# Kernel tuning notes

Hardware: AMD Instinct MI355X
Metric: run time of the kernel (lower is better)

Reference implementation:

```python
import jax, jax.numpy as jnp
import numpy as np

B, S, HID = 2, 2048, 2048
NH, NKV, DH = 16, 4, 128
EPS = 1e-6

def rotate_half(x):
    x1, x2 = x[..., : x.shape[-1] // 2], x[..., x.shape[-1] // 2 :]
    return jnp.concatenate((-x2, x1), axis=-1)

def rms_norm(x, w):
    var = jnp.mean(jnp.square(x), axis=-1, keepdims=True)
    return w * (x * jax.lax.rsqrt(var + EPS))

def setup_inputs() -> dict:
    key = jax.random.key(0)
    ks = jax.random.split(key, 8)
    hidden_states = jax.random.normal(ks[0], (B, S, HID), dtype=jnp.float32)
    # causal additive mask, broadcastable to [B, H, S, S]
    causal = jnp.tril(jnp.ones((S, S), dtype=bool))
    attention_mask = jnp.where(causal, 0.0, -1e9).astype(jnp.float32)[None, None]
    # RoPE tables: [1, S, 1, DH] to broadcast over (B, S, H, DH)
    inv_freq = 1.0 / (10000.0 ** (np.arange(0, DH, 2, dtype=np.float32) / DH))
    t = np.arange(S, dtype=np.float32)
    freqs = np.einsum('s,d->sd', t, inv_freq)
    emb = np.concatenate([freqs, freqs], axis=-1)  # [S, DH]
    cos = jnp.asarray(np.cos(emb))[None, :, None, :]
    sin = jnp.asarray(np.sin(emb))[None, :, None, :]
    std = 0.02
    Wq = jax.random.normal(ks[1], (HID, NH * DH), dtype=jnp.float32) * std
    Wk = jax.random.normal(ks[2], (HID, NKV * DH), dtype=jnp.float32) * std
    Wv = jax.random.normal(ks[3], (HID, NKV * DH), dtype=jnp.float32) * std
    Wo = jax.random.normal(ks[4], (NH * DH, HID), dtype=jnp.float32) * std
    q_norm_w = jnp.ones((DH,), dtype=jnp.float32)
    k_norm_w = jnp.ones((DH,), dtype=jnp.float32)
    return dict(hidden_states=hidden_states, attention_mask=attention_mask,
                cos=cos, sin=sin, Wq=Wq, Wk=Wk, Wv=Wv, Wo=Wo,
                q_norm_w=q_norm_w, k_norm_w=k_norm_w)

def reference(hidden_states, attention_mask, cos, sin, Wq, Wk, Wv, Wo, q_norm_w, k_norm_w):
    b, s, _ = hidden_states.shape
    q = (hidden_states @ Wq).reshape(b, s, NH, DH)
    k = (hidden_states @ Wk).reshape(b, s, NKV, DH)
    v = (hidden_states @ Wv).reshape(b, s, NKV, DH)
    # per-head RMSNorm on q/k
    q = rms_norm(q, q_norm_w)
    k = rms_norm(k, k_norm_w)
    # RoPE
    q = q * cos + rotate_half(q) * sin
    k = k * cos + rotate_half(k) * sin
    # GQA: repeat kv heads
    groups = NH // NKV
    k = jnp.repeat(k, groups, axis=2)
    v = jnp.repeat(v, groups, axis=2)
    scale = 1.0 / jnp.sqrt(jnp.asarray(DH, dtype=q.dtype))
    scores = jnp.einsum('bqhd,bkhd->bhqk', q, k) * scale  # [B,H,S,S]
    scores = scores + attention_mask
    probs = jax.nn.softmax(scores, axis=-1)
    out = jnp.einsum('bhqk,bkhd->bqhd', probs, v)
    out = out.reshape(b, s, NH * DH)
    return out @ Wo
```

## Files before the change

kernel.cpp:

```cpp
#include <hip/hip_runtime.h>
#include <hip/hip_bf16.h>
#include <stdint.h>


typedef __attribute__((ext_vector_type(8))) short short8;
typedef __attribute__((ext_vector_type(4))) float floatx4;
typedef __hip_bfloat16 bf16_t;

#define MFMA16x16(a, b, c) __builtin_amdgcn_mfma_f32_16x16x32_bf16(a, b, c, 0, 0, 0)

__device__ __forceinline__ void async_copy16(const void* g, void* l) {
  __builtin_amdgcn_global_load_lds(
      (const __attribute__((address_space(1))) void*)g,
      (__attribute__((address_space(3))) void*)l, 16, 0, 0);
}

__device__ __forceinline__ unsigned short bf16bits(float x) {
  bf16_t h = __float2bfloat16(x);
  return *reinterpret_cast<unsigned short*>(&h);
}

__global__ __launch_bounds__(256) void convbf_kernel(const float* __restrict__ in,
                                                     bf16_t* __restrict__ out, int n4) {
  int i = blockIdx.x * 256 + threadIdx.x;
  if (i < n4) {
    const float4 v = reinterpret_cast<const float4*>(in)[i];
    ushort4 o;
    o.x = bf16bits(v.x); o.y = bf16bits(v.y); o.z = bf16bits(v.z); o.w = bf16bits(v.w);
    reinterpret_cast<ushort4*>(out)[i] = o;
  }
}

__global__ __launch_bounds__(256) void wtrans_kernel(const float* __restrict__ W,
                                                     bf16_t* __restrict__ Wt, int N, int roff) {
  __shared__ float t[32][33];
  int k0 = blockIdx.y * 32, n0 = blockIdx.x * 32;
#pragma unroll
  for (int j = 0; j < 4; ++j)
    t[threadIdx.y + j * 8][threadIdx.x] =
        W[(size_t)(k0 + threadIdx.y + j * 8) * N + n0 + threadIdx.x];
  __syncthreads();
#pragma unroll
  for (int j = 0; j < 4; ++j) {
    int n = n0 + threadIdx.y + j * 8, k = k0 + threadIdx.x;
    Wt[(size_t)(roff + n) * 2048 + k] = __float2bfloat16(t[threadIdx.x][threadIdx.y + j * 8]);
  }
}

template <int OBF>
__global__ __launch_bounds__(256, 3) void gemm_bt_kernel(const bf16_t* __restrict__ A,
                                                         const bf16_t* __restrict__ Bt,
                                                         void* __restrict__ Cv,
                                                         int K, int ldc) {
  __shared__ __align__(16) char smem[32768];
  const int tid = threadIdx.x;
  const int wave = tid >> 6, lane = tid & 63;
  const int wr = wave >> 1, wc = wave & 1;
  const int l16 = lane & 15, lhi = lane >> 4;

  const int nwg = gridDim.x * gridDim.y;
  const int orig = blockIdx.y * gridDim.x + blockIdx.x;
  const int swz = (orig & 7) * (nwg >> 3) + (orig >> 3);
  const int bn = (swz % gridDim.x) * 128;
  const int bm = (swz / gridDim.x) * 128;

  floatx4 acc[4][4] = {};

  for (int k0 = 0; k0 < K; k0 += 64) {
    __syncthreads();
#pragma unroll
    for (int i = 0; i < 4; ++i) {
      int chunk = i * 4 + wave;
      unsigned p = (unsigned)chunk * 1024u + (unsigned)lane * 16u;
      unsigned row = p >> 7;
      unsigned colg = (p & 127u) ^ ((row & 7u) << 4);
      const char* gA = (const char*)(A + (size_t)(bm + row) * K + k0) + colg;
      async_copy16(gA, smem + (size_t)chunk * 1024);
      const char* gB = (const char*)(Bt + (size_t)(bn + row) * K + k0) + colg;
      async_copy16(gB, smem + 16384 + (size_t)chunk * 1024);
    }
    __syncthreads();
#pragma unroll
    for (int kk = 0; kk < 2; ++kk) {
      short8 fa[4], fb[4];
#pragma unroll
      for (int mi = 0; mi < 4; ++mi) {
        unsigned row = wr * 64 + mi * 16 + l16;
        unsigned off = row * 128u + kk * 64u + lhi * 16u;
        off ^= (row & 7u) << 4;
        fa[mi] = *(const short8*)(smem + off);
      }
#pragma unroll
      for (int ni = 0; ni < 4; ++ni) {
        unsigned row = wc * 64 + ni * 16 + l16;
        unsigned off = row * 128u + kk * 64u + lhi * 16u;
        off ^= (row & 7u) << 4;
        fb[ni] = *(const short8*)(smem + 16384 + off);
      }
#pragma unroll
      for (int mi = 0; mi < 4; ++mi)
#pragma unroll
        for (int ni = 0; ni < 4; ++ni)
          acc[mi][ni] = MFMA16x16(fa[mi], fb[ni], acc[mi][ni]);
    }
  }
#pragma unroll
  for (int mi = 0; mi < 4; ++mi)
#pragma unroll
    for (int ni = 0; ni < 4; ++ni)
#pragma unroll
      for (int r = 0; r < 4; ++r) {
        int row = bm + wr * 64 + mi * 16 + lhi * 4 + r;
        int col = bn + wc * 64 + ni * 16 + l16;
        if (OBF)
          ((bf16_t*)Cv)[(size_t)row * ldc + col] = __float2bfloat16(acc[mi][ni][r]);
        else
          ((float*)Cv)[(size_t)row * ldc + col] = acc[mi][ni][r];
      }
}

__global__ __launch_bounds__(256) void qknorm_rope_kernel(
    const bf16_t* __restrict__ Cqkv, const float* __restrict__ cosT,
    const float* __restrict__ sinT, const float* __restrict__ qw,
    const float* __restrict__ kw, bf16_t* __restrict__ Qa, bf16_t* __restrict__ Ka) {
  int wave = threadIdx.x >> 6, lane = threadIdx.x & 63;
  int task = blockIdx.x * 4 + wave;
  int unit = task % 20;
  int row = task / 20;
  int b = row >> 11, s = row & 2047;
  const bf16_t* src;
  const float* w;
  bf16_t* dst;
  float sc;
  if (unit < 16) {
    src = Cqkv + (size_t)row * 3072 + unit * 128;
    w = qw;
    dst = Qa + ((size_t)(b * 16 + unit) * 2048 + s) * 128;
    sc = 0.088388347648318447f;
  } else {
    int kh = unit - 16;
    src = Cqkv + (size_t)row * 3072 + 2048 + kh * 128;
    w = kw;
    dst = Ka + ((size_t)(b * 4 + kh) * 2048 + s) * 128;
    sc = 1.0f;
  }
  float x1 = __bfloat162float(src[lane]), x2 = __bfloat162float(src[lane + 64]);
  float ss = x1 * x1 + x2 * x2;
#pragma unroll
  for (int off = 1; off < 64; off <<= 1) ss += __shfl_xor(ss, off, 64);
  float inv = rsqrtf(ss * (1.f / 128.f) + 1e-6f);
  x1 = x1 * inv * w[lane];
  x2 = x2 * inv * w[lane + 64];
  float c1 = cosT[(size_t)s * 128 + lane], c2 = cosT[(size_t)s * 128 + lane + 64];
  float s1 = sinT[(size_t)s * 128 + lane], s2 = sinT[(size_t)s * 128 + lane + 64];
  dst[lane] = __float2bfloat16((x1 * c1 - x2 * s1) * sc);
  dst[lane + 64] = __float2bfloat16((x2 * c2 + x1 * s2) * sc);
}

__global__ __launch_bounds__(256) void vtrans_kernel(const bf16_t* __restrict__ Cqkv,
                                                     bf16_t* __restrict__ Vt) {
  __shared__ bf16_t t[32][33];
  int bk = blockIdx.z;
  int b = bk >> 2, kh = bk & 3;
  int s0 = blockIdx.x * 32, d0 = blockIdx.y * 32;
  const bf16_t* src = Cqkv + (size_t)(b * 2048) * 3072 + 2560 + kh * 128;
#pragma unroll
  for (int j = 0; j < 4; ++j)
    t[threadIdx.y + j * 8][threadIdx.x] =
        src[(size_t)(s0 + threadIdx.y + j * 8) * 3072 + d0 + threadIdx.x];
  __syncthreads();
  bf16_t* dst = Vt + (size_t)(b * 4 + kh) * 128 * 2048;
#pragma unroll
  for (int j = 0; j < 4; ++j) {
    int d = d0 + threadIdx.y + j * 8, s = s0 + threadIdx.x;
    dst[(size_t)d * 2048 + s] = t[threadIdx.x][threadIdx.y + j * 8];
  }
}

__device__ __forceinline__ unsigned swz_row(unsigned row) {
  return (((row & 7u) ^ ((row >> 3) << 1)) & 7u) << 4;
}

__global__ __launch_bounds__(256, 2) void flash_kernel(const bf16_t* __restrict__ Qa,
                                                       const bf16_t* __restrict__ Ka,
                                                       const bf16_t* __restrict__ Vt,
                                                       bf16_t* __restrict__ attnO) {
  __shared__ __align__(16) char smem[65536];
  const int tid = threadIdx.x;
  const int wave = tid >> 6, lane = tid & 63;
  const int l16 = lane & 15, lhi = lane >> 4;
  const int bid = blockIdx.x;
  const int bh = bid & 31;
  const int ib = bid >> 5;
  const int qb = (ib < 8) ? (15 - ib) : (ib - 8);
  const int h = bh & 15, b = bh >> 4;
  const int kh = h >> 2;
  const int q0b = qb << 7;
  const int q0w = q0b + wave * 32;

  const bf16_t* Qb = Qa + ((size_t)bh * 2048 + q0w) * 128;
  const bf16_t* Kb = Ka + (size_t)(b * 4 + kh) * 2048 * 128;
  const bf16_t* Vb = Vt + (size_t)(b * 4 + kh) * 128 * 2048;

  char* Kl = smem;
  char* Vl = smem + 32768;

  short8 qf[2][4];
#pragma unroll
  for (int rt = 0; rt < 2; ++rt)
#pragma unroll
    for (int kk = 0; kk < 4; ++kk)
      qf[rt][kk] = *(const short8*)(Qb + (size_t)(rt * 16 + l16) * 128 + kk * 32 + lhi * 8);

  short8 onesf;
#pragma unroll
  for (int j = 0; j < 8; ++j) onesf[j] = (short)0x3F80;

  floatx4 o[2][8] = {};
  floatx4 lsum[2] = {};
  short8 pf[2][4];
  float m[2] = {-1e30f, -1e30f};

  const float THR = 8.0f;
  const int nch = qb + 1;

  auto stageK = [&](int key0) {
#pragma unroll
    for (int it = 0; it < 8; ++it) {
      unsigned p = (unsigned)(it * 4 + wave) * 1024u + (unsigned)lane * 16u;
      unsigned row = p >> 8;
      unsigned gcol = (p & 255u) ^ swz_row(row);
      async_copy16((const char*)(Kb + (size_t)(key0 + row) * 128) + gcol,
                   Kl + (size_t)(it * 4 + wave) * 1024);
    }
  };
  auto stageV = [&](int key0) {
#pragma unroll
    for (int it = 0; it < 8; ++it) {
      unsigned p = (unsigned)(it * 4 + wave) * 1024u + (unsigned)lane * 16u;
      unsigned row = p >> 8;
      unsigned gcol = (p & 255u) ^ swz_row(row);
      async_copy16((const char*)(Vb + (size_t)row * 2048 + key0) + gcol,
                   Vl + (size_t)(it * 4 + wave) * 1024);
    }
  };

  stageK(0);
  stageV(0);
  __syncthreads();

  for (int c = 0; c < nch; ++c) {
    const int kc0 = c << 7;

    floatx4 s[2][8] = {};
    __builtin_amdgcn_s_setprio(1);
#pragma unroll
    for (int g = 0; g < 8; ++g) {
      unsigned row = (unsigned)(l16 >> 2) * 8u + (unsigned)((g & 1) * 4) +
                     (unsigned)(l16 & 3) + (unsigned)((g >> 1) * 32);
      unsigned base = row * 256u;
      unsigned px = swz_row(row);
#pragma unroll
      for (int kk = 0; kk < 4; ++kk) {
        short8 kf = *(const short8*)(Kl + base + (((unsigned)(kk * 64 + lhi * 16)) ^ px));
        s[0][g] = MFMA16x16(kf, qf[0][kk], s[0][g]);
        s[1][g] = MFMA16x16(kf, qf[1][kk], s[1][g]);
      }
    }
    __builtin_amdgcn_s_setprio(0);

    const bool needMask = (kc0 + 128 > q0w);
#pragma unroll
    for (int rt = 0; rt < 2; ++rt) {
      const int qrow = q0w + rt * 16 + l16;
      if (needMask) {
#pragma unroll
        for (int g = 0; g < 8; ++g)
#pragma unroll
          for (int r = 0; r < 4; ++r) {
            int key = kc0 + lhi * 8 + (g & 1) * 4 + r + (g >> 1) * 32;
            if (key > qrow) s[rt][g][r] = -1e9f;
          }
      }
      float mx = s[rt][0][0];
#pragma unroll
      for (int g = 0; g < 8; ++g)
#pragma unroll
        for (int r = 0; r < 4; ++r) mx = fmaxf(mx, s[rt][g][r]);
      mx = fmaxf(mx, __shfl_xor(mx, 16, 64));
      mx = fmaxf(mx, __shfl_xor(mx, 32, 64));
      bool grow = mx > m[rt] + THR;
      if (__any(grow)) {
        float mn = fmaxf(m[rt], mx);
        float corr = __expf(m[rt] - mn);
        m[rt] = mn;
#pragma unroll
        for (int r = 0; r < 4; ++r) {
          float co = __shfl(corr, lhi * 4 + r, 64);
          lsum[rt][r] *= co;
#pragma unroll
          for (int f = 0; f < 8; ++f) o[rt][f][r] *= co;
        }
      }
#pragma unroll
      for (int ks = 0; ks < 4; ++ks) {
        union { unsigned u[4]; short8 v; } pk;
#pragma unroll
        for (int half = 0; half < 2; ++half) {
          int g = ks * 2 + half;
          float p0 = __expf(s[rt][g][0] - m[rt]);
          float p1 = __expf(s[rt][g][1] - m[rt]);
          float p2 = __expf(s[rt][g][2] - m[rt]);
          float p3 = __expf(s[rt][g][3] - m[rt]);
          pk.u[half * 2] = (unsigned)bf16bits(p0) | ((unsigned)bf16bits(p1) << 16);
          pk.u[half * 2 + 1] = (unsigned)bf16bits(p2) | ((unsigned)bf16bits(p3) << 16);
        }
        pf[rt][ks] = pk.v;
      }
    }

    __syncthreads();

    if (c + 1 < nch) stageK(kc0 + 128);

    __builtin_amdgcn_s_setprio(1);
#pragma unroll
    for (int ks = 0; ks < 4; ++ks) {
#pragma unroll
      for (int f = 0; f < 8; ++f) {
        unsigned row = (unsigned)(f * 16 + l16);
        short8 vf = *(const short8*)(Vl + row * 256u +
                                     (((unsigned)(ks * 64 + lhi * 16)) ^ swz_row(row)));
        o[0][f] = MFMA16x16(pf[0][ks], vf, o[0][f]);
        o[1][f] = MFMA16x16(pf[1][ks], vf, o[1][f]);
      }
      lsum[0] = MFMA16x16(pf[0][ks], onesf, lsum[0]);
      lsum[1] = MFMA16x16(pf[1][ks], onesf, lsum[1]);
    }
    __builtin_amdgcn_s_setprio(0);

    __syncthreads();

    if (c + 1 < nch) stageV(kc0 + 128);
  }

#pragma unroll
  for (int rt = 0; rt < 2; ++rt)
#pragma unroll
    for (int r = 0; r < 4; ++r) {
      float inv = 1.f / lsum[rt][r];
      int row = q0w + rt * 16 + lhi * 4 + r;
      size_t base = ((size_t)(b * 2048) + row) * 2048 + h * 128;
#pragma unroll
      for (int f = 0; f < 8; ++f)
        attnO[base + f * 16 + l16] = __float2bfloat16(o[rt][f][r] * inv);
    }
}

extern "C" void kernel_launch(void* const* d_in, const int* in_sizes, int n_in,
                              void* d_out, int out_size, void* d_ws, size_t ws_size,
                              hipStream_t stream) {
  const float* hs = (const float*)d_in[0];
  const float* cosT = (const float*)d_in[2];
  const float* sinT = (const float*)d_in[3];
  const float* Wq = (const float*)d_in[4];
  const float* Wk = (const float*)d_in[5];
  const float* Wv = (const float*)d_in[6];
  const float* Wo = (const float*)d_in[7];
  const float* qw = (const float*)d_in[8];
  const float* kw = (const float*)d_in[9];
  float* out = (float*)d_out;

  char* ws = (char*)d_ws;
  size_t off = 0;
  auto alloc = [&](size_t bytes) {
    char* p = ws + off;
    off += (bytes + 255) & ~(size_t)255;
    return p;
  };
  bf16_t* hsb  = (bf16_t*)alloc((size_t)4096 * 2048 * 2);
  bf16_t* wqkv = (bf16_t*)alloc((size_t)3072 * 2048 * 2);
  bf16_t* wot  = (bf16_t*)alloc((size_t)2048 * 2048 * 2);
  bf16_t* cqkv = (bf16_t*)alloc((size_t)4096 * 3072 * 2);
  bf16_t* qa   = (bf16_t*)alloc((size_t)2 * 16 * 2048 * 128 * 2);
  bf16_t* ka   = (bf16_t*)alloc((size_t)2 * 4 * 2048 * 128 * 2);
  bf16_t* vt   = (bf16_t*)alloc((size_t)2 * 4 * 2048 * 128 * 2);
  bf16_t* attn = (bf16_t*)cqkv;

  convbf_kernel<<<8192, 256, 0, stream>>>(hs, hsb, 2097152);
  dim3 tb(32, 8);
  wtrans_kernel<<<dim3(64, 64), tb, 0, stream>>>(Wq, wqkv, 2048, 0);
  wtrans_kernel<<<dim3(16, 64), tb, 0, stream>>>(Wk, wqkv, 512, 2048);
  wtrans_kernel<<<dim3(16, 64), tb, 0, stream>>>(Wv, wqkv, 512, 2560);
  wtrans_kernel<<<dim3(64, 64), tb, 0, stream>>>(Wo, wot, 2048, 0);
  gemm_bt_kernel<1><<<dim3(24, 32), 256, 0, stream>>>(hsb, wqkv, cqkv, 2048, 3072);
  qknorm_rope_kernel<<<20480, 256, 0, stream>>>(cqkv, cosT, sinT, qw, kw, qa, ka);
  vtrans_kernel<<<dim3(64, 4, 8), tb, 0, stream>>>(cqkv, vt);
  flash_kernel<<<512, 256, 0, stream>>>(qa, ka, vt, attn);
  gemm_bt_kernel<0><<<dim3(16, 32), 256, 0, stream>>>(attn, wot, out, 2048, 2048);
}
```

Measured before the change: 216.5 us.

## Halve flash attention tiles to 64 queries/keys, use exp2 with folded log2e scale

The flash kernel now gives each block 64 query rows (16 per wave) and 64-key chunks, doubling the grid to 1024 blocks and halving shared memory to 32KB, with a new load-balancing map from block index to query block. The softmax scale folds in log2(e) so exponentials use the hardware exp2 directly, and the lazy-rescale threshold is raised to match the base-2 domain. This is meant to improve occupancy and load balance and cut the cost of each exponential. In exchange it halves K/V reuse per block, adds more barriers and chunk iterations, and loads more K/V in total.

After: 188.4 us (median of 2 runs). 1.15x faster.

```diff
diff --git a/kernel.cpp b/kernel.cpp
--- a/kernel.cpp
+++ b/kernel.cpp
@@ -18,6 +18,10 @@
 __device__ __forceinline__ unsigned short bf16bits(float x) {
   bf16_t h = __float2bfloat16(x);
   return *reinterpret_cast<unsigned short*>(&h);
+}
+
+__device__ __forceinline__ float fast_exp2(float x) {
+  return __builtin_amdgcn_exp2f(x);
 }
 
 __global__ __launch_bounds__(256) void convbf_kernel(const float* __restrict__ in,
@@ -136,7 +140,7 @@
     src = Cqkv + (size_t)row * 3072 + unit * 128;
     w = qw;
     dst = Qa + ((size_t)(b * 16 + unit) * 2048 + s) * 128;
-    sc = 0.088388347648318447f;
+    sc = 0.127517432f;
   } else {
     int kh = unit - 16;
     src = Cqkv + (size_t)row * 3072 + 2048 + kh * 128;
@@ -181,52 +185,53 @@
   return (((row & 7u) ^ ((row >> 3) << 1)) & 7u) << 4;
 }
 
+__device__ __constant__ unsigned char kQbMap[32] = {
+    31, 30, 29, 28, 27, 26, 25, 24,  0, 1, 2, 3, 4, 5, 6, 7,
+    23, 22, 21, 20, 19, 18, 17, 16,  8, 9, 10, 11, 12, 13, 14, 15};
+
 __global__ __launch_bounds__(256, 2) void flash_kernel(const bf16_t* __restrict__ Qa,
                                                        const bf16_t* __restrict__ Ka,
                                                        const bf16_t* __restrict__ Vt,
                                                        bf16_t* __restrict__ attnO) {
-  __shared__ __align__(16) char smem[65536];
+  __shared__ __align__(16) char smem[32768];
   const int tid = threadIdx.x;
   const int wave = tid >> 6, lane = tid & 63;
   const int l16 = lane & 15, lhi = lane >> 4;
   const int bid = blockIdx.x;
   const int bh = bid & 31;
-  const int ib = bid >> 5;
-  const int qb = (ib < 8) ? (15 - ib) : (ib - 8);
+  const int qb = kQbMap[bid >> 5];
   const int h = bh & 15, b = bh >> 4;
   const int kh = h >> 2;
-  const int q0b = qb << 7;
-  const int q0w = q0b + wave * 32;
+  const int q0b = qb << 6;
+  const int q0w = q0b + wave * 16;
 
   const bf16_t* Qb = Qa + ((size_t)bh * 2048 + q0w) * 128;
   const bf16_t* Kb = Ka + (size_t)(b * 4 + kh) * 2048 * 128;
   const bf16_t* Vb = Vt + (size_t)(b * 4 + kh) * 128 * 2048;
 
   char* Kl = smem;
-  char* Vl = smem + 32768;
-
-  short8 qf[2][4];
-#pragma unroll
-  for (int rt = 0; rt < 2; ++rt)
-#pragma unroll
-    for (int kk = 0; kk < 4; ++kk)
-      qf[rt][kk] = *(const short8*)(Qb + (size_t)(rt * 16 + l16) * 128 + kk * 32 + lhi * 8);
+  char* Vl = smem + 16384;
+
+  short8 qf[4];
+#pragma unroll
+  for (int kk = 0; kk < 4; ++kk)
+    qf[kk] = *(const short8*)(Qb + (size_t)l16 * 128 + kk * 32 + lhi * 8);
 
   short8 onesf;
 #pragma unroll
   for (int j = 0; j < 8; ++j) onesf[j] = (short)0x3F80;
 
-  floatx4 o[2][8] = {};
-  floatx4 lsum[2] = {};
-  short8 pf[2][4];
-  float m[2] = {-1e30f, -1e30f};
-
-  const float THR = 8.0f;
+  floatx4 o[8] = {};
+  floatx4 lsum = {};
+  short8 pf[2];
+  float m = -1e30f;
+
+  const float THR = 11.5f;
   const int nch = qb + 1;
 
   auto stageK = [&](int key0) {
 #pragma unroll
-    for (int it = 0; it < 8; ++it) {
+    for (int it = 0; it < 4; ++it) {
       unsigned p = (unsigned)(it * 4 + wave) * 1024u + (unsigned)lane * 16u;
       unsigned row = p >> 8;
       unsigned gcol = (p & 255u) ^ swz_row(row);
@@ -236,10 +241,10 @@
   };
   auto stageV = [&](int key0) {
 #pragma unroll
-    for (int it = 0; it < 8; ++it) {
+    for (int it = 0; it < 4; ++it) {
       unsigned p = (unsigned)(it * 4 + wave) * 1024u + (unsigned)lane * 16u;
-      unsigned row = p >> 8;
-      unsigned gcol = (p & 255u) ^ swz_row(row);
+      unsigned row = p >> 7;
+      unsigned gcol = (p & 127u) ^ swz_row(row);
       async_copy16((const char*)(Vb + (size_t)row * 2048 + key0) + gcol,
                    Vl + (size_t)(it * 4 + wave) * 1024);
     }
@@ -250,12 +255,12 @@
   __syncthreads();
 
   for (int c = 0; c < nch; ++c) {
-    const int kc0 = c << 7;
-
-    floatx4 s[2][8] = {};
+    const int kc0 = c << 6;
+
+    floatx4 s[4] = {};
     __builtin_amdgcn_s_setprio(1);
 #pragma unroll
-    for (int g = 0; g < 8; ++g) {
+    for (int g = 0; g < 4; ++g) {
       unsigned row = (unsigned)(l16 >> 2) * 8u + (unsigned)((g & 1) * 4) +
                      (unsigned)(l16 & 3) + (unsigned)((g >> 1) * 32);
       unsigned base = row * 256u;
@@ -263,98 +268,89 @@
 #pragma unroll
       for (int kk = 0; kk < 4; ++kk) {
         short8 kf = *(const short8*)(Kl + base + (((unsigned)(kk * 64 + lhi * 16)) ^ px));
-        s[0][g] = MFMA16x16(kf, qf[0][kk], s[0][g]);
-        s[1][g] = MFMA16x16(kf, qf[1][kk], s[1][g]);
+        s[g] = MFMA16x16(kf, qf[kk], s[g]);
       }
     }
     __builtin_amdgcn_s_setprio(0);
 
-    const bool needMask = (kc0 + 128 > q0w);
-#pragma unroll
-    for (int rt = 0; rt < 2; ++rt) {
-      const int qrow = q0w + rt * 16 + l16;
-      if (needMask) {
-#pragma unroll
-        for (int g = 0; g < 8; ++g)
-#pragma unroll
-          for (int r = 0; r < 4; ++r) {
-            int key = kc0 + lhi * 8 + (g & 1) * 4 + r + (g >> 1) * 32;
-            if (key > qrow) s[rt][g][r] = -1e9f;
-          }
-      }
-      float mx = s[rt][0][0];
-#pragma unroll
-      for (int g = 0; g < 8; ++g)
-#pragma unroll
-        for (int r = 0; r < 4; ++r) mx = fmaxf(mx, s[rt][g][r]);
-      mx = fmaxf(mx, __shfl_xor(mx, 16, 64));
-      mx = fmaxf(mx, __shfl_xor(mx, 32, 64));
-      bool grow = mx > m[rt] + THR;
-      if (__any(grow)) {
-        float mn = fmaxf(m[rt], mx);
-        float corr = __expf(m[rt] - mn);
-        m[rt] = mn;
+    const int qrow = q0w + l16;
+    if (kc0 + 64 > q0w) {
+#pragma unroll
+      for (int g = 0; g < 4; ++g)
 #pragma unroll
         for (int r = 0; r < 4; ++r) {
-          float co = __shfl(corr, lhi * 4 + r, 64);
-          lsum[rt][r] *= co;
-#pragma unroll
-          for (int f = 0; f < 8; ++f) o[rt][f][r] *= co;
+          int key = kc0 + lhi * 8 + (g & 1) * 4 + r + (g >> 1) * 32;
+          if (key > qrow) s[g][r] = -1e9f;
         }
-      }
-#pragma unroll
-      for (int ks = 0; ks < 4; ++ks) {
-        union { unsigned u[4]; short8 v; } pk;
-#pragma unroll
-        for (int half = 0; half < 2; ++half) {
-          int g = ks * 2 + half;
-          float p0 = __expf(s[rt][g][0] - m[rt]);
-          float p1 = __expf(s[rt][g][1] - m[rt]);
-          float p2 = __expf(s[rt][g][2] - m[rt]);
-          float p3 = __expf(s[rt][g][3] - m[rt]);
-          pk.u[half * 2] = (unsigned)bf16bits(p0) | ((unsigned)bf16bits(p1) << 16);
-          pk.u[half * 2 + 1] = (unsigned)bf16bits(p2) | ((unsigned)bf16bits(p3) << 16);
-        }
-        pf[rt][ks] = pk.v;
-      }
+    }
+    float m0 = fmaxf(fmaxf(s[0][0], s[0][1]), fmaxf(s[0][2], s[0][3]));
+    float m1 = fmaxf(fmaxf(s[1][0], s[1][1]), fmaxf(s[1][2], s[1][3]));
+    float m2 = fmaxf(fmaxf(s[2][0], s[2][1]), fmaxf(s[2][2], s[2][3]));
+    float m3 = fmaxf(fmaxf(s[3][0], s[3][1]), fmaxf(s[3][2], s[3][3]));
+    float mx = fmaxf(fmaxf(m0, m1), fmaxf(m2, m3));
+    mx = fmaxf(mx, __shfl_xor(mx, 16, 64));
+    mx = fmaxf(mx, __shfl_xor(mx, 32, 64));
+    bool grow = mx > m + THR;
+    if (__any(grow)) {
+      float mn = fmaxf(m, mx);
+      float corr = fast_exp2(m - mn);
+      m = mn;
+#pragma unroll
+      for (int r = 0; r < 4; ++r) {
+        float co = __shfl(corr, lhi * 4 + r, 64);
+        lsum[r] *= co;
+#pragma unroll
+        for (int f = 0; f < 8; ++f) o[f][r] *= co;
+      }
+    }
+#pragma unroll
+    for (int ks = 0; ks < 2; ++ks) {
+      union { unsigned u[4]; short8 v; } pk;
+#pragma unroll
+      for (int half = 0; half < 2; ++half) {
+        int g = ks * 2 + half;
+        float p0 = fast_exp2(s[g][0] - m);
+        float p1 = fast_exp2(s[g][1] - m);
+        float p2 = fast_exp2(s[g][2] - m);
+        float p3 = fast_exp2(s[g][3] - m);
+        pk.u[half * 2] = (unsigned)bf16bits(p0) | ((unsigned)bf16bits(p1) << 16);
+        pk.u[half * 2 + 1] = (unsigned)bf16bits(p2) | ((unsigned)bf16bits(p3) << 16);
+      }
+      pf[ks] = pk.v;
     }
 
     __syncthreads();
 
-    if (c + 1 < nch) stageK(kc0 + 128);
+    if (c + 1 < nch) stageK((c + 1) << 6);
 
     __builtin_amdgcn_s_setprio(1);
 #pragma unroll
-    for (int ks = 0; ks < 4; ++ks) {
+    for (int ks = 0; ks < 2; ++ks) {
 #pragma unroll
       for (int f = 0; f < 8; ++f) {
         unsigned row = (unsigned)(f * 16 + l16);
-        short8 vf = *(const short8*)(Vl + row * 256u +
+        short8 vf = *(const short8*)(Vl + row * 128u +
                                      (((unsigned)(ks * 64 + lhi * 16)) ^ swz_row(row)));
-        o[0][f] = MFMA16x16(pf[0][ks], vf, o[0][f]);
-        o[1][f] = MFMA16x16(pf[1][ks], vf, o[1][f]);
-      }
-      lsum[0] = MFMA16x16(pf[0][ks], onesf, lsum[0]);
-      lsum[1] = MFMA16x16(pf[1][ks], onesf, lsum[1]);
+        o[f] = MFMA16x16(pf[ks], vf, o[f]);
+      }
+      lsum = MFMA16x16(pf[ks], onesf, lsum);
     }
     __builtin_amdgcn_s_setprio(0);
 
     __syncthreads();
 
-    if (c + 1 < nch) stageV(kc0 + 128);
-  }
-
-#pragma unroll
-  for (int rt = 0; rt < 2; ++rt)
-#pragma unroll
-    for (int r = 0; r < 4; ++r) {
-      float inv = 1.f / lsum[rt][r];
-      int row = q0w + rt * 16 + lhi * 4 + r;
-      size_t base = ((size_t)(b * 2048) + row) * 2048 + h * 128;
-#pragma unroll
-      for (int f = 0; f < 8; ++f)
-        attnO[base + f * 16 + l16] = __float2bfloat16(o[rt][f][r] * inv);
-    }
+    if (c + 1 < nch) stageV((c + 1) << 6);
+  }
+
+#pragma unroll
+  for (int r = 0; r < 4; ++r) {
+    float inv = 1.f / lsum[r];
+    int row = q0w + lhi * 4 + r;
+    size_t base = ((size_t)(b * 2048) + row) * 2048 + h * 128;
+#pragma unroll
+    for (int f = 0; f < 8; ++f)
+      attnO[base + f * 16 + l16] = __float2bfloat16(o[f][r] * inv);
+  }
 }
 
 extern "C" void kernel_launch(void* const* d_in, const int* in_sizes, int n_in,
@@ -396,6 +392,6 @@
   gemm_bt_kernel<1><<<dim3(24, 32), 256, 0, stream>>>(hsb, wqkv, cqkv, 2048, 3072);
   qknorm_rope_kernel<<<20480, 256, 0, stream>>>(cqkv, cosT, sinT, qw, kw, qa, ka);
   vtrans_kernel<<<dim3(64, 4, 8), tb, 0, stream>>>(cqkv, vt);
-  flash_kernel<<<512, 256, 0, stream>>>(qa, ka, vt, attn);
+  flash_kernel<<<1024, 256, 0, stream>>>(qa, ka, vt, attn);
   gemm_bt_kernel<0><<<dim3(16, 32), 256, 0, stream>>>(attn, wot, out, 2048, 2048);
 }
```
